# Optimization experiments

Hardware: AMD Instinct MI355X
Metric: run time of the kernel (lower is better)

## Reference

```python
import jax, jax.numpy as jnp
import numpy as np

N = 1_000_000
E = 1_000_000
K = 512
H = 64
F_IN = 19
N_ITERS = 3
EPS = 1e-5

def _leaky(x):
    return jax.nn.leaky_relu(x, negative_slope=0.01)

def _layernorm(x, g, b):
    mu = jnp.mean(x, axis=-1, keepdims=True)
    var = jnp.var(x, axis=-1, keepdims=True)
    return (x - mu) * jax.lax.rsqrt(var + EPS) * g + b

def setup_inputs() -> dict:
    key = jax.random.key(0)
    ks = jax.random.split(key, 20)
    s = 0.1
    inp = {
        "x": jax.random.normal(ks[0], (N, F_IN), dtype=jnp.float32),
        "edge_index": jax.random.randint(ks[1], (2, E), 0, N, dtype=jnp.int64),
        "candidate_indices": jax.random.randint(ks[2], (K,), 0, N, dtype=jnp.int64),
        # embedding params
        "pW_in": jax.random.normal(ks[3], (F_IN, H), dtype=jnp.float32) * s,
        "pb_in": jnp.zeros((H,), dtype=jnp.float32),
        "eW": jax.random.normal(ks[4], (2, H, H), dtype=jnp.float32) * s,
        "eb": jnp.zeros((2, H), dtype=jnp.float32),
        "gamma": jnp.ones((2, H), dtype=jnp.float32),
        "beta": jnp.zeros((2, H), dtype=jnp.float32),
        # bottom-up step MLPs (stacked over n_iters)
        "sW1": jax.random.normal(ks[5], (N_ITERS, H, H), dtype=jnp.float32) * s,
        "sb1": jnp.zeros((N_ITERS, H), dtype=jnp.float32),
        "sW2": jax.random.normal(ks[6], (N_ITERS, H, H), dtype=jnp.float32) * s,
        "sb2": jnp.zeros((N_ITERS, H), dtype=jnp.float32),
        # score head
        "hW1": jax.random.normal(ks[7], (H, H), dtype=jnp.float32) * s,
        "hb1": jnp.zeros((H,), dtype=jnp.float32),
        "hW2": jax.random.normal(ks[8], (H, 1), dtype=jnp.float32) * s,
        "hb2": jnp.zeros((1,), dtype=jnp.float32),
    }
    return inp

def reference(x, edge_index, candidate_indices, pW_in, pb_in, eW, eb, gamma, beta,
              sW1, sb1, sW2, sb2, hW1, hb1, hW2, hb2):
    # TreeNodeEmbedding: proj + 2 residual layers with LayerNorm
    h = _leaky(x @ pW_in + pb_in)
    for i in range(2):
        h = _layernorm(h + _leaky(h @ eW[i] + eb[i]), gamma[i], beta[i])
    parent_idx = edge_index[0]
    child_idx = edge_index[1]
    # Bottom-up message passing: scatter-mean over children, tiny MLP update
    for i in range(N_ITERS):
        child_h = h[child_idx]                                   # [E, H] gather
        sum_p = jax.ops.segment_sum(child_h, parent_idx, num_segments=N)  # [N, H]
        cnt = jax.ops.segment_sum(jnp.ones((E,), dtype=h.dtype), parent_idx, num_segments=N)  # [N]
        mean_p = sum_p / jnp.maximum(cnt, 1.0)[:, None]
        mask = (cnt > 0)[:, None]
        delta = _leaky(mean_p @ sW1[i] + sb1[i]) @ sW2[i] + sb2[i]
        h = h + jnp.where(mask, delta, 0.0)
    # Score head on candidates, softmax over k (all candidates real -> full_logits == scores)
    cand_h = h[candidate_indices]                                # [K, H]
    scores = (_leaky(cand_h @ hW1 + hb1) @ hW2 + hb2)[:, 0]      # [K]
    probs = jax.nn.softmax(scores)
    return probs
```

## Files before the change

kernel.cpp:

```cpp
#include <hip/hip_runtime.h>
#include <hip/hip_bf16.h>
#include <math.h>

#define H 64
#define FIN 19
#define EPSLN 1e-5f

#define TB 1024
#define NWV 16
#define NBLK 128

#define OFF_PW   0
#define OFF_PB   1280
#define OFF_EW   1344
#define OFF_EB   9536
#define OFF_G    9664
#define OFF_BT   9792
#define OFF_W1   9920
#define OFF_W2   22208
#define OFF_B1   34496
#define OFF_B2   34688
#define OFF_HW1  34880
#define OFF_HB1  38976
#define OFF_HW2  39040
#define OFF_HB2  39104
#define WTS_TOTAL 39105

__device__ __forceinline__ float leaky(float v) { return v > 0.f ? v : 0.01f * v; }

__device__ __forceinline__ float wsumf(float v) {
#pragma unroll
  for (int off = 32; off > 0; off >>= 1) v += __shfl_xor(v, off, 64);
  return v;
}

__device__ __forceinline__ void wsync() {
  asm volatile("" ::: "memory");
  __builtin_amdgcn_wave_barrier();
  asm volatile("" ::: "memory");
}

__device__ __forceinline__ bool detect_bf16(const unsigned short* xs) {
  const int lane = threadIdx.x & 63;
  unsigned a = xs[lane], b = xs[64 + lane];
  unsigned ea = (a >> 7) & 0xFFu, ebx = (b >> 7) & 0xFFu;
  return !__any((int)(ea > 140u || ebx > 140u));
}

__device__ __forceinline__ bool detect_i64(const int* w) {
  const int lane = threadIdx.x & 63;
  return __all((int)(w[2 * lane + 1] == 0));
}

__device__ __forceinline__ float ldf(const void* p, size_t i, bool bf) {
  return bf ? __bfloat162float(((const __hip_bfloat16*)p)[i]) : ((const float*)p)[i];
}

struct WT {
  const void* src[14];
  int off[14], len[14], sl[14], rp[14], rs[14], cs[14];
};

__device__ __forceinline__ void prep_one(const WT& T, bool bf, float* wts, int i) {
  int p = 0;
  while (i >= T.off[p] + T.len[p]) ++p;
  const int loc = i - T.off[p];
  float v;
  if (T.rp[p] == 0) {
    v = ldf(T.src[p], loc, bf);
  } else {
    const int s = loc / T.sl[p];
    const int r = loc - s * T.sl[p];
    const int j = r / T.rp[p];
    const int k = r - j * T.rp[p];
    v = (k < T.rs[p])
            ? ldf(T.src[p], (size_t)s * T.rs[p] * T.cs[p] + (size_t)k * T.cs[p] + j, bf)
            : 0.f;
  }
  wts[i] = v;
}

__global__ __launch_bounds__(256) void prep_wts(WT T, const unsigned short* xs,
                                                float* wts, int total) {
  const bool bf = detect_bf16(xs);
  for (int i = blockIdx.x * 256 + threadIdx.x; i < total; i += gridDim.x * 256)
    prep_one(T, bf, wts, i);
}

__device__ float embed_math(const void* x, const float* wts, float* stg, int v,
                            int lane, bool bf) {
  float xv = (lane < FIN) ? ldf(x, (size_t)v * FIN + lane, bf) : 0.f;
  wsync();
  stg[lane] = xv;
  wsync();
  const float* tp = wts + OFF_PW + lane * 20;
  float a0 = wts[OFF_PB + lane], a1 = 0.f, a2 = 0.f, a3 = 0.f;
#pragma unroll
  for (int k = 0; k < 20; k += 4) {
    float4 m = *(const float4*)&stg[k];
    float4 w = *(const float4*)&tp[k];
    a0 += m.x * w.x; a1 += m.y * w.y; a2 += m.z * w.z; a3 += m.w * w.w;
  }
  float h = leaky((a0 + a1) + (a2 + a3));
#pragma unroll
  for (int L = 0; L < 2; ++L) {
    wsync();
    stg[lane] = h;
    wsync();
    const float* tw = wts + OFF_EW + L * 4096 + lane * 64;
    a0 = wts[OFF_EB + L * 64 + lane]; a1 = a2 = a3 = 0.f;
#pragma unroll
    for (int k = 0; k < H; k += 4) {
      float4 m = *(const float4*)&stg[k];
      float4 w = *(const float4*)&tw[k];
      a0 += m.x * w.x; a1 += m.y * w.y; a2 += m.z * w.z; a3 += m.w * w.w;
    }
    float val = h + leaky((a0 + a1) + (a2 + a3));
    float mu = wsumf(val) * (1.f / 64.f);
    float d = val - mu;
    float var = wsumf(d * d) * (1.f / 64.f);
    h = d * (1.f / sqrtf(var + EPSLN)) * wts[OFF_G + L * 64 + lane] +
        wts[OFF_BT + L * 64 + lane];
  }
  return h;
}

__device__ float delta_math(const float* wts, float* stg, float mean, int it, int lane) {
  wsync();
  stg[lane] = mean;
  wsync();
  const float* w1 = wts + OFF_W1 + it * 4096 + lane * 64;
  float a0 = wts[OFF_B1 + it * 64 + lane], a1 = 0.f, a2 = 0.f, a3 = 0.f;
#pragma unroll
  for (int k = 0; k < H; k += 4) {
    float4 m = *(const float4*)&stg[k];
    float4 w = *(const float4*)&w1[k];
    a0 += m.x * w.x; a1 += m.y * w.y; a2 += m.z * w.z; a3 += m.w * w.w;
  }
  float t1 = leaky((a0 + a1) + (a2 + a3));
  wsync();
  stg[lane] = t1;
  wsync();
  const float* w2 = wts + OFF_W2 + it * 4096 + lane * 64;
  a0 = wts[OFF_B2 + it * 64 + lane]; a1 = a2 = a3 = 0.f;
#pragma unroll
  for (int k = 0; k < H; k += 4) {
    float4 m = *(const float4*)&stg[k];
    float4 w = *(const float4*)&w2[k];
    a0 += m.x * w.x; a1 += m.y * w.y; a2 += m.z * w.z; a3 += m.w * w.w;
  }
  wsync();
  return (a0 + a1) + (a2 + a3);
}

__device__ float score_math(const float* wts, float* stg, float hv, int lane) {
  wsync();
  stg[lane] = hv;
  wsync();
  const float* hw1 = wts + OFF_HW1 + lane * 64;
  float a0 = wts[OFF_HB1 + lane], a1 = 0.f, a2 = 0.f, a3 = 0.f;
#pragma unroll
  for (int k = 0; k < H; k += 4) {
    float4 m = *(const float4*)&stg[k];
    float4 w = *(const float4*)&hw1[k];
    a0 += m.x * w.x; a1 += m.y * w.y; a2 += m.z * w.z; a3 += m.w * w.w;
  }
  wsync();
  float t1 = leaky((a0 + a1) + (a2 + a3));
  return wsumf(t1 * wts[OFF_HW2 + lane]) + wts[OFF_HB2];
}

__global__ __launch_bounds__(256) void init_kernel(int* map, int nN, int* counters, int K,
                                                   int* ch3, int n3, int* ch2, int n2,
                                                   int* ch1, int n1) {
  const int tid = blockIdx.x * 256 + threadIdx.x;
  const int stride = gridDim.x * 256;
  for (int i = tid; i < nN; i += stride) map[i] = 0;
  for (int i = tid; i < n3; i += stride) ch3[i] = -1;
  for (int i = tid; i < n2; i += stride) ch2[i] = -1;
  for (int i = tid; i < n1; i += stride) ch1[i] = -1;
  if (tid < 3) counters[tid] = 0;
  if (tid == 3) counters[3] = K;
}

__global__ __launch_bounds__(64) void seed_kernel(const int* cand_raw, int K, int nN,
                                                  int* map, int* node3, int* nextSame3,
                                                  int* selfChild3, int* ctr2, int cap2,
                                                  int* node2) {
  const bool i64 = detect_i64(cand_raw);
  int t = blockIdx.x * 64 + threadIdx.x;
  if (t >= K) return;
  int cv = i64 ? cand_raw[2 * t] : cand_raw[t];
  unsigned n = (unsigned)cv;
  if (n >= (unsigned)nN) n = 0;
  node3[t] = (int)n;
  int enc = (1 << 24) | t;
  int old = atomicExch(&map[n], enc);
  nextSame3[t] = ((old >> 24) == 1) ? (old & 0xFFFFFF) : -1;
  int s = atomicAdd(ctr2, 1);
  if (s < cap2) { node2[s] = (int)n; selfChild3[t] = s; } else selfChild3[t] = 0;
}

__global__ __launch_bounds__(256) void regself_kernel(const int* ctrU_, int capU,
                                                      const int* nodeU, int* map, int epoch,
                                                      int* nextSameU, int* ctrD, int capD,
                                                      int* nodeD, int* selfChildU) {
  int cnt = *ctrU_; if (cnt > capU) cnt = capU;
  int t = blockIdx.x * 256 + threadIdx.x;
  if (t >= cnt) return;
  int n = nodeU[t];
  int enc = (epoch << 24) | t;
  int old = atomicExch(&map[n], enc);
  nextSameU[t] = ((old >> 24) == epoch) ? (old & 0xFFFFFF) : -1;
  int s = atomicAdd(ctrD, 1);
  if (s < capD) { nodeD[s] = n; selfChildU[t] = s; } else selfChildU[t] = 0;
}

__global__ __launch_bounds__(256) void scan_kernel(const int* eraw, int E, int nN,
                                                   const int* map, int epoch,
                                                   const int* nextSameU, int* childHeadU,
                                                   int* ctrD, int capD, int* nodeD,
                                                   int* childNextD) {
  const bool i64 = detect_i64(eraw);
  int e = blockIdx.x * 256 + threadIdx.x;
  if (e >= E) return;
  int pv = i64 ? eraw[2 * e] : eraw[e];
  unsigned p = (unsigned)pv;
  if (p >= (unsigned)nN) p = 0;
  int m = map[p];
  if ((m >> 24) != epoch) return;
  int cv = i64 ? eraw[2 * (E + e)] : eraw[E + e];
  unsigned c = (unsigned)cv;
  if (c >= (unsigned)nN) c = 0;
  int t = m & 0xFFFFFF;
  while (t >= 0) {
    int ct = atomicAdd(ctrD, 1);
    if (ct < capD) {
      nodeD[ct] = (int)c;
      childNextD[ct] = atomicExch(&childHeadU[t], ct);
    }
    t = nextSameU[t];
  }
}

__global__ __launch_bounds__(64) void eval0_kernel(const void* x, const int* ctr0_,
                                                   int cap0, const int* node0,
                                                   const float* wts, float* val0) {
  __shared__ float stg[H];
  int cnt = *ctr0_; if (cnt > cap0) cnt = cap0;
  const int t = blockIdx.x;
  if (t >= cnt) return;
  const int lane = threadIdx.x;
  const bool bf = detect_bf16((const unsigned short*)x);
  float h = embed_math(x, wts, stg, node0[t], lane, bf);
  val0[(size_t)t * H + lane] = h;
}

__global__ __launch_bounds__(64) void evalL_kernel(const int* ctrU_, int capU,
                                                   const int* selfChildU,
                                                   const int* childHeadU,
                                                   const int* childNextD,
                                                   const float* valD, float* valU,
                                                   const float* wts, int it) {
  __shared__ float stg[H];
  int cnt = *ctrU_; if (cnt > capU) cnt = capU;
  const int t = blockIdx.x;
  if (t >= cnt) return;
  const int lane = threadIdx.x;
  float hv = valD[(size_t)selfChildU[t] * H + lane];
  float acc = 0.f;
  int k = 0;
  int c = childHeadU[t];
  while (c >= 0) { acc += valD[(size_t)c * H + lane]; ++k; c = childNextD[c]; }
  if (k > 0) hv += delta_math(wts, stg, acc / (float)k, it, lane);
  valU[(size_t)t * H + lane] = hv;
}

__global__ __launch_bounds__(512) void score_kernel(
    const float* __restrict__ candH, const float* __restrict__ wts,
    const void* x, void* out, int K) {
  __shared__ float red[512];
  const int t = threadIdx.x;
  const bool bf = detect_bf16((const unsigned short*)x);
  float sc = 0.f;
  if (t < K) {
    float hr[H];
#pragma unroll
    for (int k = 0; k < H; k += 4) {
      float4 v = *(const float4*)&candH[(size_t)t * H + k];
      hr[k] = v.x; hr[k + 1] = v.y; hr[k + 2] = v.z; hr[k + 3] = v.w;
    }
    for (int j = 0; j < H; ++j) {
      float a = wts[OFF_HB1 + j];
#pragma unroll
      for (int k = 0; k < H; k += 4) {
        float4 w = *(const float4*)&wts[OFF_HW1 + j * 64 + k];
        a += hr[k] * w.x + hr[k + 1] * w.y + hr[k + 2] * w.z + hr[k + 3] * w.w;
      }
      sc += leaky(a) * wts[OFF_HW2 + j];
    }
    sc += wts[OFF_HB2];
  }
  red[t] = (t < K) ? sc : -3.0e38f;
  __syncthreads();
  for (int off = 256; off > 0; off >>= 1) {
    if (t < off) red[t] = fmaxf(red[t], red[t + off]);
    __syncthreads();
  }
  const float m = red[0];
  __syncthreads();
  const float ex = (t < K) ? expf(sc - m) : 0.f;
  red[t] = ex;
  __syncthreads();
  for (int off = 256; off > 0; off >>= 1) {
    if (t < off) red[t] += red[t + off];
    __syncthreads();
  }
  const float inv = 1.f / red[0];
  if (t < K) {
    float p = ex * inv;
    if (bf) ((__hip_bfloat16*)out)[t] = __float2bfloat16(p);
    else    ((float*)out)[t] = p;
  }
}

struct FA {
  const void* x; const void* edge; const void* cand; void* outp;
  int nN, E, K, CAP2, CAP1, CAP0;
  int *ctrl;
  int *map3, *map2, *map1;
  int *chHead3, *chHead2, *chHead1;
  float* wts;
  int *node3, *nextSame3, *selfCh3;
  int *node2, *nextSame2, *selfCh2, *chNext2;
  int *node1, *nextSame1, *selfCh1, *chNext1;
  int *node0, *chNext0;
  float *val0, *val1, *val2, *scores;
  WT T;
};

#define CLINE 32

__device__ __forceinline__ void gsync(int* ctrl, int& phase) {
  __syncthreads();
  if (threadIdx.x == 0) {
    ++phase;
    const int nB = (int)gridDim.x;
    const int clu = (int)blockIdx.x >> 5;
    const int nClu = (nB + 31) >> 5;
    int cluSize = nB - (clu << 5);
    if (cluSize > 32) cluSize = 32;
    int old = __hip_atomic_fetch_add(&ctrl[clu * CLINE], 1, __ATOMIC_ACQ_REL,
                                     __HIP_MEMORY_SCOPE_AGENT);
    if (old == phase * cluSize - 1) {
      int mold = __hip_atomic_fetch_add(&ctrl[64 * CLINE], 1, __ATOMIC_ACQ_REL,
                                        __HIP_MEMORY_SCOPE_AGENT);
      if (mold == phase * nClu - 1) {
#pragma unroll
        for (int f = 0; f < 32; ++f)
          __hip_atomic_store(&ctrl[(65 + f) * CLINE], phase, __ATOMIC_RELEASE,
                             __HIP_MEMORY_SCOPE_AGENT);
      }
    }
    int* myFlag = &ctrl[(65 + ((int)blockIdx.x & 31)) * CLINE];
    int guard = 0;
    while (__hip_atomic_load(myFlag, __ATOMIC_RELAXED,
                             __HIP_MEMORY_SCOPE_AGENT) < phase) {
      __builtin_amdgcn_s_sleep(2);
      if (++guard > (1 << 21)) break;
    }
    (void)__hip_atomic_load(myFlag, __ATOMIC_ACQUIRE, __HIP_MEMORY_SCOPE_AGENT);
  }
  __syncthreads();
}

__global__ __launch_bounds__(TB, 4) void fused_kernel(FA A) {
  __shared__ float smem[NWV * H];
  const int tid = threadIdx.x;
  const int lane = tid & 63;
  const int wib = tid >> 6;
  const int gtid = blockIdx.x * TB + tid;
  const int nthr = (int)gridDim.x * TB;
  const int waveId = blockIdx.x * NWV + wib;
  const int nWaves = (int)gridDim.x * NWV;
  float* stg = &smem[wib * H];
  int* ctrl = A.ctrl;
  int* c2 = &ctrl[97 * CLINE];
  int* c1 = &ctrl[98 * CLINE];
  int* c0 = &ctrl[99 * CLINE];
  int phase = 0;

  const bool bf = detect_bf16((const unsigned short*)A.x);
  const int* eraw = (const int*)A.edge;
  const int* craw = (const int*)A.cand;
  const bool i64e = detect_i64(eraw);
  const bool i64c = detect_i64(craw);

  for (int i = gtid; i < A.nN; i += nthr) {
    A.map3[i] = -1; A.map2[i] = -1; A.map1[i] = -1;
  }
  for (int i = gtid; i < A.K; i += nthr) A.chHead3[i] = -1;
  for (int i = gtid; i < A.CAP2; i += nthr) A.chHead2[i] = -1;
  for (int i = gtid; i < A.CAP1; i += nthr) A.chHead1[i] = -1;
  gsync(ctrl, phase);

  for (int i = gtid; i < WTS_TOTAL; i += nthr) prep_one(A.T, bf, A.wts, i);
  for (int t = gtid; t < A.K; t += nthr) {
    int cv = i64c ? craw[2 * t] : craw[t];
    unsigned n = (unsigned)cv;
    if (n >= (unsigned)A.nN) n = 0;
    A.node3[t] = (int)n;
    A.nextSame3[t] = atomicExch(&A.map3[(int)n], t);
    int s = atomicAdd(c2, 1);
    if (s < A.CAP2) {
      A.node2[s] = (int)n; A.selfCh3[t] = s;
      A.nextSame2[s] = atomicExch(&A.map2[(int)n], s);
      int s1 = atomicAdd(c1, 1);
      if (s1 < A.CAP1) {
        A.node1[s1] = (int)n; A.selfCh2[s] = s1;
        A.nextSame1[s1] = atomicExch(&A.map1[(int)n], s1);
        int s0 = atomicAdd(c0, 1);
        if (s0 < A.CAP0) { A.node0[s0] = (int)n; A.selfCh1[s1] = s0; }
        else A.selfCh1[s1] = 0;
      } else A.selfCh2[s] = 0;
    } else A.selfCh3[t] = 0;
  }
  gsync(ctrl, phase);

  for (int e = gtid; e < A.E; e += nthr) {
    int pv = i64e ? eraw[2 * e] : eraw[e];
    unsigned p = (unsigned)pv;
    if (p >= (unsigned)A.nN) p = 0;
    int t = A.map3[p];
    if (t < 0) continue;
    int cv = i64e ? eraw[2 * (A.E + e)] : eraw[A.E + e];
    unsigned cn = (unsigned)cv;
    if (cn >= (unsigned)A.nN) cn = 0;
    for (; t >= 0; t = A.nextSame3[t]) {
      int ct = atomicAdd(c2, 1);
      if (ct < A.CAP2) {
        A.node2[ct] = (int)cn;
        A.chNext2[ct] = atomicExch(&A.chHead3[t], ct);
        A.nextSame2[ct] = atomicExch(&A.map2[(int)cn], ct);
        int s1 = atomicAdd(c1, 1);
        if (s1 < A.CAP1) {
          A.node1[s1] = (int)cn; A.selfCh2[ct] = s1;
          A.nextSame1[s1] = atomicExch(&A.map1[(int)cn], s1);
          int s0 = atomicAdd(c0, 1);
          if (s0 < A.CAP0) { A.node0[s0] = (int)cn; A.selfCh1[s1] = s0; }
          else A.selfCh1[s1] = 0;
        } else A.selfCh2[ct] = 0;
      }
    }
  }
  gsync(ctrl, phase);

  for (int e = gtid; e < A.E; e += nthr) {
    int pv = i64e ? eraw[2 * e] : eraw[e];
    unsigned p = (unsigned)pv;
    if (p >= (unsigned)A.nN) p = 0;
    int t = A.map2[p];
    if (t < 0) continue;
    int cv = i64e ? eraw[2 * (A.E + e)] : eraw[A.E + e];
    unsigned cn = (unsigned)cv;
    if (cn >= (unsigned)A.nN) cn = 0;
    for (; t >= 0; t = A.nextSame2[t]) {
      int ct = atomicAdd(c1, 1);
      if (ct < A.CAP1) {
        A.node1[ct] = (int)cn;
        A.chNext1[ct] = atomicExch(&A.chHead2[t], ct);
        A.nextSame1[ct] = atomicExch(&A.map1[(int)cn], ct);
        int s0 = atomicAdd(c0, 1);
        if (s0 < A.CAP0) { A.node0[s0] = (int)cn; A.selfCh1[ct] = s0; }
        else A.selfCh1[ct] = 0;
      }
    }
  }
  gsync(ctrl, phase);

  for (int e = gtid; e < A.E; e += nthr) {
    int pv = i64e ? eraw[2 * e] : eraw[e];
    unsigned p = (unsigned)pv;
    if (p >= (unsigned)A.nN) p = 0;
    int t = A.map1[p];
    if (t < 0) continue;
    int cv = i64e ? eraw[2 * (A.E + e)] : eraw[A.E + e];
    unsigned cn = (unsigned)cv;
    if (cn >= (unsigned)A.nN) cn = 0;
    for (; t >= 0; t = A.nextSame1[t]) {
      int ct = atomicAdd(c0, 1);
      if (ct < A.CAP0) {
        A.node0[ct] = (int)cn;
        A.chNext0[ct] = atomicExch(&A.chHead1[t], ct);
      }
    }
  }
  gsync(ctrl, phase);

  {
    int cnt = __hip_atomic_load(c0, __ATOMIC_RELAXED, __HIP_MEMORY_SCOPE_AGENT);
    if (cnt > A.CAP0) cnt = A.CAP0;
    for (int t = waveId; t < cnt; t += nWaves) {
      float h = embed_math(A.x, A.wts, stg, A.node0[t], lane, bf);
      A.val0[(size_t)t * H + lane] = h;
    }
  }
  gsync(ctrl, phase);

  {
    int cnt = __hip_atomic_load(c1, __ATOMIC_RELAXED, __HIP_MEMORY_SCOPE_AGENT);
    if (cnt > A.CAP1) cnt = A.CAP1;
    for (int t = waveId; t < cnt; t += nWaves) {
      float hv = A.val0[(size_t)A.selfCh1[t] * H + lane];
      float acc = 0.f;
      int kc = 0;
      for (int c = A.chHead1[t]; c >= 0; c = A.chNext0[c]) {
        acc += A.val0[(size_t)c * H + lane];
        ++kc;
      }
      if (kc > 0) hv += delta_math(A.wts, stg, acc / (float)kc, 0, lane);
      A.val1[(size_t)t * H + lane] = hv;
    }
  }
  gsync(ctrl, phase);

  {
    int cnt = __hip_atomic_load(c2, __ATOMIC_RELAXED, __HIP_MEMORY_SCOPE_AGENT);
    if (cnt > A.CAP2) cnt = A.CAP2;
    for (int t = waveId; t < cnt; t += nWaves) {
      float hv = A.val1[(size_t)A.selfCh2[t] * H + lane];
      float acc = 0.f;
      int kc = 0;
      for (int c = A.chHead2[t]; c >= 0; c = A.chNext1[c]) {
        acc += A.val1[(size_t)c * H + lane];
        ++kc;
      }
      if (kc > 0) hv += delta_math(A.wts, stg, acc / (float)kc, 1, lane);
      A.val2[(size_t)t * H + lane] = hv;
    }
  }
  gsync(ctrl, phase);

  for (int t = waveId; t < A.K; t += nWaves) {
    float hv = A.val2[(size_t)A.selfCh3[t] * H + lane];
    float acc = 0.f;
    int kc = 0;
    for (int c = A.chHead3[t]; c >= 0; c = A.chNext2[c]) {
      acc += A.val2[(size_t)c * H + lane];
      ++kc;
    }
    if (kc > 0) hv += delta_math(A.wts, stg, acc / (float)kc, 2, lane);
    float sc = score_math(A.wts, stg, hv, lane);
    if (lane == 0) A.scores[t] = sc;
  }
  gsync(ctrl, phase);

  if (blockIdx.x == 0) {
    __shared__ float red[TB];
    float lm = -3.0e38f;
    for (int i = tid; i < A.K; i += TB) lm = fmaxf(lm, A.scores[i]);
    red[tid] = lm;
    __syncthreads();
    for (int off = TB / 2; off > 0; off >>= 1) {
      if (tid < off) red[tid] = fmaxf(red[tid], red[tid + off]);
      __syncthreads();
    }
    const float m = red[0];
    __syncthreads();
    float ls = 0.f;
    for (int i = tid; i < A.K; i += TB) {
      float e = expf(A.scores[i] - m);
      A.scores[i] = e;
      ls += e;
    }
    red[tid] = ls;
    __syncthreads();
    for (int off = TB / 2; off > 0; off >>= 1) {
      if (tid < off) red[tid] += red[tid + off];
      __syncthreads();
    }
    const float inv = 1.f / red[0];
    for (int i = tid; i < A.K; i += TB) {
      float pv = A.scores[i] * inv;
      if (bf) ((__hip_bfloat16*)A.outp)[i] = __float2bfloat16(pv);
      else    ((float*)A.outp)[i] = pv;
    }
  }
}

extern "C" void kernel_launch(void* const* d_in, const int* in_sizes, int n_in,
                              void* d_out, int out_size, void* d_ws, size_t ws_size,
                              hipStream_t stream) {
  const void* x   = d_in[0];
  const int* edge = (const int*)d_in[1];
  const int* cand = (const int*)d_in[2];
  const int nN = in_sizes[0] / FIN;
  const int E  = in_sizes[1] / 2;
  const int K  = in_sizes[2];

  if (K > 2048 || K < 128 || E < 128 || nN < 1) return;

  const int CAP2 = 8 * K, CAP1 = 16 * K, CAP0 = 32 * K;

  auto al = [](size_t b) -> size_t { return (b + 255) & ~(size_t)255; };
  const size_t szW   = (size_t)WTS_TOTAL * sizeof(float);
  const size_t szMap = (size_t)nN * sizeof(int);
  const size_t szK   = (size_t)K * sizeof(int);
  const size_t sz2   = (size_t)CAP2 * sizeof(int);
  const size_t sz1   = (size_t)CAP1 * sizeof(int);
  const size_t sz0   = (size_t)CAP0 * sizeof(int);
  const size_t szV0  = (size_t)CAP0 * H * sizeof(float);
  const size_t szV1  = (size_t)CAP1 * H * sizeof(float);
  const size_t szV2  = (size_t)CAP2 * H * sizeof(float);
  const size_t szV3  = (size_t)K * H * sizeof(float);
  const size_t szCtrl = 16384;

  WT T;
  auto setv = [&](int i, const void* s, int o, int l) {
    T.src[i] = s; T.off[i] = o; T.len[i] = l; T.sl[i] = l;
    T.rp[i] = 0; T.rs[i] = 0; T.cs[i] = 0;
  };
  auto setm = [&](int i, const void* s, int o, int l, int sl, int rpad, int rs, int cs) {
    T.src[i] = s; T.off[i] = o; T.len[i] = l; T.sl[i] = sl;
    T.rp[i] = rpad; T.rs[i] = rs; T.cs[i] = cs;
  };
  setm(0,  d_in[3],  OFF_PW,  1280, 1280, 20, 19, 64);
  setv(1,  d_in[4],  OFF_PB,  64);
  setm(2,  d_in[5],  OFF_EW,  8192, 4096, 64, 64, 64);
  setv(3,  d_in[6],  OFF_EB,  128);
  setv(4,  d_in[7],  OFF_G,   128);
  setv(5,  d_in[8],  OFF_BT,  128);
  setm(6,  d_in[9],  OFF_W1,  12288, 4096, 64, 64, 64);
  setm(7,  d_in[11], OFF_W2,  12288, 4096, 64, 64, 64);
  setv(8,  d_in[10], OFF_B1,  192);
  setv(9,  d_in[12], OFF_B2,  192);
  setm(10, d_in[13], OFF_HW1, 4096, 4096, 64, 64, 64);
  setv(11, d_in[14], OFF_HB1, 64);
  setv(12, d_in[15], OFF_HW2, 64);
  setv(13, d_in[16], OFF_HB2, 1);

  int dev = 0, nCU = 0, maxB = 0;
  bool okq = (hipGetDevice(&dev) == hipSuccess) &&
             (hipDeviceGetAttribute(&nCU, hipDeviceAttributeMultiprocessorCount,
                                    dev) == hipSuccess) &&
             (hipOccupancyMaxActiveBlocksPerMultiprocessor(&maxB, fused_kernel, TB,
                                                           0) == hipSuccess) &&
             nCU >= 8 && maxB >= 1;

  const size_t needF = al(szCtrl) + 3 * al(szMap) + al(szK) + al(sz2) + al(sz1) +
                       al(szW) + 3 * al(szK) + 4 * al(sz2) + 4 * al(sz1) +
                       2 * al(sz0) + al(szV0) + al(szV1) + al(szV2) + al(szK);

  if (okq && ws_size >= needF) {
    char* wsb = (char*)d_ws;
    size_t off = 0;
    auto carve = [&](size_t bytes) -> void* {
      void* p = wsb + off;
      off += (bytes + 255) & ~(size_t)255;
      return p;
    };
    FA A;
    A.x = x; A.edge = edge; A.cand = cand; A.outp = d_out;
    A.nN = nN; A.E = E; A.K = K; A.CAP2 = CAP2; A.CAP1 = CAP1; A.CAP0 = CAP0;
    A.ctrl = (int*)carve(szCtrl);
    A.map3 = (int*)carve(szMap);
    A.map2 = (int*)carve(szMap);
    A.map1 = (int*)carve(szMap);
    A.chHead3 = (int*)carve(szK);
    A.chHead2 = (int*)carve(sz2);
    A.chHead1 = (int*)carve(sz1);
    A.wts = (float*)carve(szW);
    A.node3 = (int*)carve(szK); A.nextSame3 = (int*)carve(szK); A.selfCh3 = (int*)carve(szK);
    A.node2 = (int*)carve(sz2); A.nextSame2 = (int*)carve(sz2);
    A.selfCh2 = (int*)carve(sz2); A.chNext2 = (int*)carve(sz2);
    A.node1 = (int*)carve(sz1); A.nextSame1 = (int*)carve(sz1);
    A.selfCh1 = (int*)carve(sz1); A.chNext1 = (int*)carve(sz1);
    A.node0 = (int*)carve(sz0); A.chNext0 = (int*)carve(sz0);
    A.val0 = (float*)carve(szV0); A.val1 = (float*)carve(szV1);
    A.val2 = (float*)carve(szV2);
    A.scores = (float*)carve(szK);
    A.T = T;

    int g = NBLK;
    if (g > nCU * maxB) g = nCU * maxB;
    if (g >= 8) {
      hipMemsetAsync(A.ctrl, 0, szCtrl, stream);
      fused_kernel<<<g, TB, 0, stream>>>(A);
      return;
    }
  }

  {
    const size_t need = al(szW) + al(szMap) + 256 +
                        4 * al(szK) + 5 * al(sz2) + 5 * al(sz1) + 2 * al(sz0) +
                        al(szV0) + al(szV1) + al(szV2) + al(szV3);
    if (ws_size < need) return;

    char* wsb = (char*)d_ws;
    size_t off = 0;
    auto carve = [&](size_t bytes) -> void* {
      void* p = wsb + off;
      off += (bytes + 255) & ~(size_t)255;
      return p;
    };
    float* wts     = (float*)carve(szW);
    int* map       = (int*)carve(szMap);
    int* counters  = (int*)carve(256);
    int* node3     = (int*)carve(szK);
    int* nextSame3 = (int*)carve(szK);
    int* selfCh3   = (int*)carve(szK);
    int* chHead3   = (int*)carve(szK);
    int* node2     = (int*)carve(sz2);
    int* nextSame2 = (int*)carve(sz2);
    int* selfCh2   = (int*)carve(sz2);
    int* chHead2   = (int*)carve(sz2);
    int* chNext2   = (int*)carve(sz2);
    int* node1     = (int*)carve(sz1);
    int* nextSame1 = (int*)carve(sz1);
    int* selfCh1   = (int*)carve(sz1);
    int* chHead1   = (int*)carve(sz1);
    int* chNext1   = (int*)carve(sz1);
    int* node0     = (int*)carve(sz0);
    int* chNext0   = (int*)carve(sz0);
    float* val0    = (float*)carve(szV0);
    float* val1    = (float*)carve(szV1);
    float* val2    = (float*)carve(szV2);
    float* val3    = (float*)carve(szV3);

    prep_wts<<<160, 256, 0, stream>>>(T, (const unsigned short*)x, wts, WTS_TOTAL);
    init_kernel<<<1024, 256, 0, stream>>>(map, nN, counters, K, chHead3, K,
                                          chHead2, CAP2, chHead1, CAP1);
    seed_kernel<<<(K + 63) / 64, 64, 0, stream>>>(cand, K, nN, map, node3, nextSame3,
                                                  selfCh3, &counters[0], CAP2, node2);
    scan_kernel<<<(E + 255) / 256, 256, 0, stream>>>(edge, E, nN, map, 1, nextSame3,
                                                     chHead3, &counters[0], CAP2,
                                                     node2, chNext2);
    regself_kernel<<<(CAP2 + 255) / 256, 256, 0, stream>>>(&counters[0], CAP2, node2, map, 2,
                                                           nextSame2, &counters[1], CAP1,
                                                           node1, selfCh2);
    scan_kernel<<<(E + 255) / 256, 256, 0, stream>>>(edge, E, nN, map, 2, nextSame2,
                                                     chHead2, &counters[1], CAP1,
                                                     node1, chNext1);
    regself_kernel<<<(CAP1 + 255) / 256, 256, 0, stream>>>(&counters[1], CAP1, node1, map, 3,
                                                           nextSame1, &counters[2], CAP0,
                                                           node0, selfCh1);
    scan_kernel<<<(E + 255) / 256, 256, 0, stream>>>(edge, E, nN, map, 3, nextSame1,
                                                     chHead1, &counters[2], CAP0,
                                                     node0, chNext0);

    eval0_kernel<<<CAP0, 64, 0, stream>>>(x, &counters[2], CAP0, node0, wts, val0);
    evalL_kernel<<<CAP1, 64, 0, stream>>>(&counters[1], CAP1, selfCh1, chHead1, chNext0,
                                          val0, val1, wts, 0);
    evalL_kernel<<<CAP2, 64, 0, stream>>>(&counters[0], CAP2, selfCh2, chHead2, chNext1,
                                          val1, val2, wts, 1);
    evalL_kernel<<<K, 64, 0, stream>>>(&counters[3], K, selfCh3, chHead3, chNext2,
                                       val2, val3, wts, 2);

    score_kernel<<<1, 512, 0, stream>>>(val3, wts, x, d_out, K);
  }
}
```

Baseline: 272.3 us.

## Drop init grid barrier, relax gsync atomics, double persistent grid size

The in-kernel -1 initialization of map and child-head arrays, and the grid barrier after it, are replaced by a host-side 0xFF memset issued before launch. The grid barrier's acquire/release atomics are relaxed to plain relaxed ordering with compiler fences, and cross-block writes now use relaxed agent-scope atomic stores. Unused node2/node1/node3 arrays are removed, and the persistent grid grows from 128 to 256 blocks. This saves one global barrier and some stores, but relying on relaxed ordering without proper fences risks memory-visibility races between phases, and the shorter spin guard could let a block leave a barrier early.

```diff
diff --git a/kernel.cpp b/kernel.cpp
--- a/kernel.cpp
+++ b/kernel.cpp
@@ -8,7 +8,7 @@
 
 #define TB 1024
 #define NWV 16
-#define NBLK 128
+#define NBLK 256
 
 #define OFF_PW   0
 #define OFF_PB   1280
@@ -34,6 +34,14 @@
   return v;
 }
 
+template <typename T>
+__device__ __forceinline__ void cst(T* p, T v) {
+  __hip_atomic_store(p, v, __ATOMIC_RELAXED, __HIP_MEMORY_SCOPE_AGENT);
+}
+__device__ __forceinline__ int cld(const int* p) {
+  return __hip_atomic_load(p, __ATOMIC_RELAXED, __HIP_MEMORY_SCOPE_AGENT);
+}
+
 __device__ __forceinline__ void wsync() {
   asm volatile("" ::: "memory");
   __builtin_amdgcn_wave_barrier();
@@ -77,7 +85,7 @@
             ? ldf(T.src[p], (size_t)s * T.rs[p] * T.cs[p] + (size_t)k * T.cs[p] + j, bf)
             : 0.f;
   }
-  wts[i] = v;
+  cst(&wts[i], v);
 }
 
 __global__ __launch_bounds__(256) void prep_wts(WT T, const unsigned short* xs,
@@ -331,9 +339,9 @@
   int *map3, *map2, *map1;
   int *chHead3, *chHead2, *chHead1;
   float* wts;
-  int *node3, *nextSame3, *selfCh3;
-  int *node2, *nextSame2, *selfCh2, *chNext2;
-  int *node1, *nextSame1, *selfCh1, *chNext1;
+  int *nextSame3, *selfCh3;
+  int *nextSame2, *selfCh2, *chNext2;
+  int *nextSame1, *selfCh1, *chNext1;
   int *node0, *chNext0;
   float *val0, *val1, *val2, *scores;
   WT T;
@@ -350,15 +358,16 @@
     const int nClu = (nB + 31) >> 5;
     int cluSize = nB - (clu << 5);
     if (cluSize > 32) cluSize = 32;
-    int old = __hip_atomic_fetch_add(&ctrl[clu * CLINE], 1, __ATOMIC_ACQ_REL,
+    asm volatile("" ::: "memory");
+    int old = __hip_atomic_fetch_add(&ctrl[clu * CLINE], 1, __ATOMIC_RELAXED,
                                      __HIP_MEMORY_SCOPE_AGENT);
     if (old == phase * cluSize - 1) {
-      int mold = __hip_atomic_fetch_add(&ctrl[64 * CLINE], 1, __ATOMIC_ACQ_REL,
+      int mold = __hip_atomic_fetch_add(&ctrl[64 * CLINE], 1, __ATOMIC_RELAXED,
                                         __HIP_MEMORY_SCOPE_AGENT);
       if (mold == phase * nClu - 1) {
 #pragma unroll
         for (int f = 0; f < 32; ++f)
-          __hip_atomic_store(&ctrl[(65 + f) * CLINE], phase, __ATOMIC_RELEASE,
+          __hip_atomic_store(&ctrl[(65 + f) * CLINE], phase, __ATOMIC_RELAXED,
                              __HIP_MEMORY_SCOPE_AGENT);
       }
     }
@@ -367,9 +376,9 @@
     while (__hip_atomic_load(myFlag, __ATOMIC_RELAXED,
                              __HIP_MEMORY_SCOPE_AGENT) < phase) {
       __builtin_amdgcn_s_sleep(2);
-      if (++guard > (1 << 21)) break;
-    }
-    (void)__hip_atomic_load(myFlag, __ATOMIC_ACQUIRE, __HIP_MEMORY_SCOPE_AGENT);
+      if (++guard > (1 << 18)) break;
+    }
+    asm volatile("" ::: "memory");
   }
   __syncthreads();
 }
@@ -396,34 +405,25 @@
   const bool i64e = detect_i64(eraw);
   const bool i64c = detect_i64(craw);
 
-  for (int i = gtid; i < A.nN; i += nthr) {
-    A.map3[i] = -1; A.map2[i] = -1; A.map1[i] = -1;
-  }
-  for (int i = gtid; i < A.K; i += nthr) A.chHead3[i] = -1;
-  for (int i = gtid; i < A.CAP2; i += nthr) A.chHead2[i] = -1;
-  for (int i = gtid; i < A.CAP1; i += nthr) A.chHead1[i] = -1;
-  gsync(ctrl, phase);
-
   for (int i = gtid; i < WTS_TOTAL; i += nthr) prep_one(A.T, bf, A.wts, i);
   for (int t = gtid; t < A.K; t += nthr) {
     int cv = i64c ? craw[2 * t] : craw[t];
     unsigned n = (unsigned)cv;
     if (n >= (unsigned)A.nN) n = 0;
-    A.node3[t] = (int)n;
-    A.nextSame3[t] = atomicExch(&A.map3[(int)n], t);
+    cst(&A.nextSame3[t], atomicExch(&A.map3[(int)n], t));
     int s = atomicAdd(c2, 1);
     if (s < A.CAP2) {
-      A.node2[s] = (int)n; A.selfCh3[t] = s;
-      A.nextSame2[s] = atomicExch(&A.map2[(int)n], s);
+      cst(&A.selfCh3[t], s);
+      cst(&A.nextSame2[s], atomicExch(&A.map2[(int)n], s));
       int s1 = atomicAdd(c1, 1);
       if (s1 < A.CAP1) {
-        A.node1[s1] = (int)n; A.selfCh2[s] = s1;
-        A.nextSame1[s1] = atomicExch(&A.map1[(int)n], s1);
+        cst(&A.selfCh2[s], s1);
+        cst(&A.nextSame1[s1], atomicExch(&A.map1[(int)n], s1));
         int s0 = atomicAdd(c0, 1);
-        if (s0 < A.CAP0) { A.node0[s0] = (int)n; A.selfCh1[s1] = s0; }
-        else A.selfCh1[s1] = 0;
-      } else A.selfCh2[s] = 0;
-    } else A.selfCh3[t] = 0;
+        if (s0 < A.CAP0) { cst(&A.node0[s0], (int)n); cst(&A.selfCh1[s1], s0); }
+        else cst(&A.selfCh1[s1], 0);
+      } else cst(&A.selfCh2[s], 0);
+    } else cst(&A.selfCh3[t], 0);
   }
   gsync(ctrl, phase);
 
@@ -439,17 +439,16 @@
     for (; t >= 0; t = A.nextSame3[t]) {
       int ct = atomicAdd(c2, 1);
       if (ct < A.CAP2) {
-        A.node2[ct] = (int)cn;
-        A.chNext2[ct] = atomicExch(&A.chHead3[t], ct);
-        A.nextSame2[ct] = atomicExch(&A.map2[(int)cn], ct);
+        cst(&A.chNext2[ct], atomicExch(&A.chHead3[t], ct));
+        cst(&A.nextSame2[ct], atomicExch(&A.map2[(int)cn], ct));
         int s1 = atomicAdd(c1, 1);
         if (s1 < A.CAP1) {
-          A.node1[s1] = (int)cn; A.selfCh2[ct] = s1;
-          A.nextSame1[s1] = atomicExch(&A.map1[(int)cn], s1);
+          cst(&A.selfCh2[ct], s1);
+          cst(&A.nextSame1[s1], atomicExch(&A.map1[(int)cn], s1));
           int s0 = atomicAdd(c0, 1);
-          if (s0 < A.CAP0) { A.node0[s0] = (int)cn; A.selfCh1[s1] = s0; }
-          else A.selfCh1[s1] = 0;
-        } else A.selfCh2[ct] = 0;
+          if (s0 < A.CAP0) { cst(&A.node0[s0], (int)cn); cst(&A.selfCh1[s1], s0); }
+          else cst(&A.selfCh1[s1], 0);
+        } else cst(&A.selfCh2[ct], 0);
       }
     }
   }
@@ -467,12 +466,11 @@
     for (; t >= 0; t = A.nextSame2[t]) {
       int ct = atomicAdd(c1, 1);
       if (ct < A.CAP1) {
-        A.node1[ct] = (int)cn;
-        A.chNext1[ct] = atomicExch(&A.chHead2[t], ct);
-        A.nextSame1[ct] = atomicExch(&A.map1[(int)cn], ct);
+        cst(&A.chNext1[ct], atomicExch(&A.chHead2[t], ct));
+        cst(&A.nextSame1[ct], atomicExch(&A.map1[(int)cn], ct));
         int s0 = atomicAdd(c0, 1);
-        if (s0 < A.CAP0) { A.node0[s0] = (int)cn; A.selfCh1[ct] = s0; }
-        else A.selfCh1[ct] = 0;
+        if (s0 < A.CAP0) { cst(&A.node0[s0], (int)cn); cst(&A.selfCh1[ct], s0); }
+        else cst(&A.selfCh1[ct], 0);
       }
     }
   }
@@ -490,25 +488,25 @@
     for (; t >= 0; t = A.nextSame1[t]) {
       int ct = atomicAdd(c0, 1);
       if (ct < A.CAP0) {
-        A.node0[ct] = (int)cn;
-        A.chNext0[ct] = atomicExch(&A.chHead1[t], ct);
+        cst(&A.node0[ct], (int)cn);
+        cst(&A.chNext0[ct], atomicExch(&A.chHead1[t], ct));
       }
     }
   }
   gsync(ctrl, phase);
 
   {
-    int cnt = __hip_atomic_load(c0, __ATOMIC_RELAXED, __HIP_MEMORY_SCOPE_AGENT);
+    int cnt = cld(c0);
     if (cnt > A.CAP0) cnt = A.CAP0;
     for (int t = waveId; t < cnt; t += nWaves) {
       float h = embed_math(A.x, A.wts, stg, A.node0[t], lane, bf);
-      A.val0[(size_t)t * H + lane] = h;
+      cst(&A.val0[(size_t)t * H + lane], h);
     }
   }
   gsync(ctrl, phase);
 
   {
-    int cnt = __hip_atomic_load(c1, __ATOMIC_RELAXED, __HIP_MEMORY_SCOPE_AGENT);
+    int cnt = cld(c1);
     if (cnt > A.CAP1) cnt = A.CAP1;
     for (int t = waveId; t < cnt; t += nWaves) {
       float hv = A.val0[(size_t)A.selfCh1[t] * H + lane];
@@ -519,13 +517,13 @@
         ++kc;
       }
       if (kc > 0) hv += delta_math(A.wts, stg, acc / (float)kc, 0, lane);
-      A.val1[(size_t)t * H + lane] = hv;
+      cst(&A.val1[(size_t)t * H + lane], hv);
     }
   }
   gsync(ctrl, phase);
 
   {
-    int cnt = __hip_atomic_load(c2, __ATOMIC_RELAXED, __HIP_MEMORY_SCOPE_AGENT);
+    int cnt = cld(c2);
     if (cnt > A.CAP2) cnt = A.CAP2;
     for (int t = waveId; t < cnt; t += nWaves) {
       float hv = A.val1[(size_t)A.selfCh2[t] * H + lane];
@@ -536,7 +534,7 @@
         ++kc;
       }
       if (kc > 0) hv += delta_math(A.wts, stg, acc / (float)kc, 1, lane);
-      A.val2[(size_t)t * H + lane] = hv;
+      cst(&A.val2[(size_t)t * H + lane], hv);
     }
   }
   gsync(ctrl, phase);
@@ -551,7 +549,7 @@
     }
     if (kc > 0) hv += delta_math(A.wts, stg, acc / (float)kc, 2, lane);
     float sc = score_math(A.wts, stg, hv, lane);
-    if (lane == 0) A.scores[t] = sc;
+    if (lane == 0) cst(&A.scores[t], sc);
   }
   gsync(ctrl, phase);
 
@@ -648,7 +646,7 @@
              nCU >= 8 && maxB >= 1;
 
   const size_t needF = al(szCtrl) + 3 * al(szMap) + al(szK) + al(sz2) + al(sz1) +
-                       al(szW) + 3 * al(szK) + 4 * al(sz2) + 4 * al(sz1) +
+                       al(szW) + 2 * al(szK) + 3 * al(sz2) + 3 * al(sz1) +
                        2 * al(sz0) + al(szV0) + al(szV1) + al(szV2) + al(szK);
 
   if (okq && ws_size >= needF) {
@@ -663,18 +661,20 @@
     A.x = x; A.edge = edge; A.cand = cand; A.outp = d_out;
     A.nN = nN; A.E = E; A.K = K; A.CAP2 = CAP2; A.CAP1 = CAP1; A.CAP0 = CAP0;
     A.ctrl = (int*)carve(szCtrl);
+    char* ffs = wsb + off;
     A.map3 = (int*)carve(szMap);
     A.map2 = (int*)carve(szMap);
     A.map1 = (int*)carve(szMap);
     A.chHead3 = (int*)carve(szK);
     A.chHead2 = (int*)carve(sz2);
     A.chHead1 = (int*)carve(sz1);
+    const size_t ffbytes = (size_t)((wsb + off) - ffs);
     A.wts = (float*)carve(szW);
-    A.node3 = (int*)carve(szK); A.nextSame3 = (int*)carve(szK); A.selfCh3 = (int*)carve(szK);
-    A.node2 = (int*)carve(sz2); A.nextSame2 = (int*)carve(sz2);
-    A.selfCh2 = (int*)carve(sz2); A.chNext2 = (int*)carve(sz2);
-    A.node1 = (int*)carve(sz1); A.nextSame1 = (int*)carve(sz1);
-    A.selfCh1 = (int*)carve(sz1); A.chNext1 = (int*)carve(sz1);
+    A.nextSame3 = (int*)carve(szK); A.selfCh3 = (int*)carve(szK);
+    A.nextSame2 = (int*)carve(sz2); A.selfCh2 = (int*)carve(sz2);
+    A.chNext2 = (int*)carve(sz2);
+    A.nextSame1 = (int*)carve(sz1); A.selfCh1 = (int*)carve(sz1);
+    A.chNext1 = (int*)carve(sz1);
     A.node0 = (int*)carve(sz0); A.chNext0 = (int*)carve(sz0);
     A.val0 = (float*)carve(szV0); A.val1 = (float*)carve(szV1);
     A.val2 = (float*)carve(szV2);
@@ -683,8 +683,10 @@
 
     int g = NBLK;
     if (g > nCU * maxB) g = nCU * maxB;
+    if (g > 2048) g = 2048;
     if (g >= 8) {
       hipMemsetAsync(A.ctrl, 0, szCtrl, stream);
+      hipMemsetAsync(ffs, 0xFF, ffbytes, stream);
       fused_kernel<<<g, TB, 0, stream>>>(A);
       return;
     }
```

After: 269.1 us. No clear change (-1.2%).
